# Kernel optimization log

Hardware: AMD Instinct MI355X
Metric: run time of the kernel (lower is better)

Reference implementation:

```python
import jax, jax.numpy as jnp
import numpy as np

B, T, E = 2, 2048, 1024
H = 16            # num_heads (global in source repo)
D = E // H        # head_len
LN_EPS = 1e-5


def setup_inputs() -> dict:
    key = jax.random.key(0)
    ks = jax.random.split(key, 12)
    s = lambda fan_in: 1.0 / np.sqrt(fan_in)
    return {
        "x":     jax.random.normal(ks[0], (B, T, E), jnp.float32),
        "ln1_g": jnp.ones((E,), jnp.float32),
        "ln1_b": jnp.zeros((E,), jnp.float32),
        "Wq":    jax.random.normal(ks[1], (E, E), jnp.float32) * s(E),
        "Wk":    jax.random.normal(ks[2], (E, E), jnp.float32) * s(E),
        "Wv":    jax.random.normal(ks[3], (E, E), jnp.float32) * s(E),
        "Wo":    jax.random.normal(ks[4], (E, E), jnp.float32) * s(E),
        "bo":    jnp.zeros((E,), jnp.float32),
        "ln2_g": jnp.ones((E,), jnp.float32),
        "ln2_b": jnp.zeros((E,), jnp.float32),
        "W1":    jax.random.normal(ks[5], (E, 4 * E), jnp.float32) * s(E),
        "b1":    jnp.zeros((4 * E,), jnp.float32),
        "W2":    jax.random.normal(ks[6], (4 * E, E), jnp.float32) * s(4 * E),
        "b2":    jnp.zeros((E,), jnp.float32),
    }


def _layernorm(x, g, b):
    mu = jnp.mean(x, axis=-1, keepdims=True)
    var = jnp.mean(jnp.square(x - mu), axis=-1, keepdims=True)
    return (x - mu) * jax.lax.rsqrt(var + LN_EPS) * g + b


def _attention(x, Wq, Wk, Wv, Wo, bo):
    b, t, e = x.shape
    q = (x @ Wq).reshape(b, t, H, D)
    k = (x @ Wk).reshape(b, t, H, D)
    v = (x @ Wv).reshape(b, t, H, D)
    scores = jnp.einsum("bqhd,bkhd->bhqk", q, k) / np.sqrt(D).astype(np.float32)
    causal = jnp.tril(jnp.ones((t, t), bool))
    scores = jnp.where(causal, scores, -jnp.inf)
    attn = jax.nn.softmax(scores, axis=-1)
    out = jnp.einsum("bhqk,bkhd->bqhd", attn, v).reshape(b, t, e)
    return out @ Wo + bo


def reference(x, ln1_g, ln1_b, Wq, Wk, Wv, Wo, bo, ln2_g, ln2_b, W1, b1, W2, b2):
    # pre-norm attention + residual (dropout=0 / eval mode)
    x = x + _attention(_layernorm(x, ln1_g, ln1_b), Wq, Wk, Wv, Wo, bo)
    # pre-norm MLP + residual
    h = _layernorm(x, ln2_g, ln2_b)
    h = jax.nn.relu(h @ W1 + b1) @ W2 + b2
    return x + h
```

## Files before the change

### kernel.cpp

```cpp
#include <hip/hip_runtime.h>
#include <cmath>
#include <cstdint>
#include <cstddef>

typedef __bf16 bf16_t;
typedef _Float16 f16_t;
typedef __bf16 bf16x8 __attribute__((ext_vector_type(8)));
typedef float  f32x4  __attribute__((ext_vector_type(4)));

#define B_   2
#define T_   2048
#define E_   1024
#define H_   16
#define D_   64
#define FF_  4096
#define NROW (B_ * T_)
#define QS_  (3 * E_)
#define NTI  (T_ / 64)

__device__ __forceinline__ float4 ld4h(const f16_t* p)
{
    union { ushort4 u; f16_t h[4]; } c;
    c.u = *(const ushort4*)p;
    return make_float4((float)c.h[0], (float)c.h[1], (float)c.h[2], (float)c.h[3]);
}

__global__ __launch_bounds__(256) void ln_kernel(
    const float* __restrict__ x, const float* __restrict__ g,
    const float* __restrict__ bta, bf16_t* __restrict__ out)
{
    int row = blockIdx.x;
    int tid = threadIdx.x;
    const float4* xr = (const float4*)(x + (size_t)row * E_);
    float4 v = xr[tid];
    float s  = v.x + v.y + v.z + v.w;
    float ss = v.x * v.x + v.y * v.y + v.z * v.z + v.w * v.w;
#pragma unroll
    for (int off = 32; off; off >>= 1) {
        s  += __shfl_xor(s, off);
        ss += __shfl_xor(ss, off);
    }
    __shared__ float red[8];
    int wave = tid >> 6, lane = tid & 63;
    if (lane == 0) { red[wave] = s; red[4 + wave] = ss; }
    __syncthreads();
    s  = red[0] + red[1] + red[2] + red[3];
    ss = red[4] + red[5] + red[6] + red[7];
    float mu   = s * (1.0f / E_);
    float var  = ss * (1.0f / E_) - mu * mu;
    float rstd = rsqrtf(var + 1e-5f);
    float4 gv = ((const float4*)g)[tid];
    float4 bv = ((const float4*)bta)[tid];
    union { bf16_t h[4]; ushort4 u; } pk;
    pk.h[0] = (bf16_t)((v.x - mu) * rstd * gv.x + bv.x);
    pk.h[1] = (bf16_t)((v.y - mu) * rstd * gv.y + bv.y);
    pk.h[2] = (bf16_t)((v.z - mu) * rstd * gv.z + bv.z);
    pk.h[3] = (bf16_t)((v.w - mu) * rstd * gv.w + bv.w);
    ((ushort4*)(out + (size_t)row * E_))[tid] = pk.u;
}

__global__ __launch_bounds__(256) void ln_reduce2(
    const f16_t* __restrict__ p, const float* __restrict__ bias,
    const float* __restrict__ resid, float* __restrict__ x1,
    const float* __restrict__ g, const float* __restrict__ bta,
    bf16_t* __restrict__ out)
{
    int row = blockIdx.x;
    int tid = threadIdx.x;
    size_t off = (size_t)row * E_;
    float4 v0 = ld4h(p + off + tid * 4);
    float4 v1 = ld4h(p + (size_t)NROW * E_ + off + tid * 4);
    float4 bb = ((const float4*)bias)[tid];
    float4 rr = ((const float4*)(resid + off))[tid];
    float4 v;
    v.x = v0.x + v1.x + bb.x + rr.x;
    v.y = v0.y + v1.y + bb.y + rr.y;
    v.z = v0.z + v1.z + bb.z + rr.z;
    v.w = v0.w + v1.w + bb.w + rr.w;
    ((float4*)(x1 + off))[tid] = v;
    float s  = v.x + v.y + v.z + v.w;
    float ss = v.x * v.x + v.y * v.y + v.z * v.z + v.w * v.w;
#pragma unroll
    for (int o = 32; o; o >>= 1) {
        s  += __shfl_xor(s, o);
        ss += __shfl_xor(ss, o);
    }
    __shared__ float red[8];
    int wave = tid >> 6, lane = tid & 63;
    if (lane == 0) { red[wave] = s; red[4 + wave] = ss; }
    __syncthreads();
    s  = red[0] + red[1] + red[2] + red[3];
    ss = red[4] + red[5] + red[6] + red[7];
    float mu   = s * (1.0f / E_);
    float var  = ss * (1.0f / E_) - mu * mu;
    float rstd = rsqrtf(var + 1e-5f);
    float4 gv = ((const float4*)g)[tid];
    float4 bv = ((const float4*)bta)[tid];
    union { bf16_t h[4]; ushort4 u; } pk;
    pk.h[0] = (bf16_t)((v.x - mu) * rstd * gv.x + bv.x);
    pk.h[1] = (bf16_t)((v.y - mu) * rstd * gv.y + bv.y);
    pk.h[2] = (bf16_t)((v.z - mu) * rstd * gv.z + bv.z);
    pk.h[3] = (bf16_t)((v.w - mu) * rstd * gv.w + bv.w);
    ((ushort4*)(out + off))[tid] = pk.u;
}

__global__ __launch_bounds__(256) void add_reduce4(
    const f16_t* __restrict__ p, const float* __restrict__ bias,
    const float* __restrict__ resid, float* __restrict__ out)
{
    int row = blockIdx.x;
    int tid = threadIdx.x;
    size_t off = (size_t)row * E_ + tid * 4;
    const size_t MN = (size_t)NROW * E_;
    float4 v0 = ld4h(p + off);
    float4 v1 = ld4h(p + MN + off);
    float4 v2 = ld4h(p + 2 * MN + off);
    float4 v3 = ld4h(p + 3 * MN + off);
    float4 bb = ((const float4*)bias)[tid];
    float4 rr = ((const float4*)(resid + (size_t)row * E_))[tid];
    float4 v;
    v.x = (v0.x + v1.x) + (v2.x + v3.x) + bb.x + rr.x;
    v.y = (v0.y + v1.y) + (v2.y + v3.y) + bb.y + rr.y;
    v.z = (v0.z + v1.z) + (v2.z + v3.z) + bb.z + rr.z;
    v.w = (v0.w + v1.w) + (v2.w + v3.w) + bb.w + rr.w;
    ((float4*)(out + (size_t)row * E_))[tid] = v;
}

__global__ __launch_bounds__(256) void transpose_all(
    const float* __restrict__ Wq, const float* __restrict__ Wk,
    const float* __restrict__ Wv, const float* __restrict__ Wo,
    const float* __restrict__ W1, const float* __restrict__ W2,
    bf16_t* __restrict__ wqkv, bf16_t* __restrict__ wot,
    bf16_t* __restrict__ w1t, bf16_t* __restrict__ w2t)
{
    int l = blockIdx.x;
    const float* W; bf16_t* Wt; int K, N, bx, by;
    if (l < 4096) {
        int seg = l >> 10, r = l & 1023;
        K = E_; N = E_; bx = r & 31; by = r >> 5;
        if      (seg == 0) { W = Wq; Wt = wqkv; }
        else if (seg == 1) { W = Wk; Wt = wqkv + (size_t)E_ * E_; }
        else if (seg == 2) { W = Wv; Wt = wqkv + (size_t)2 * E_ * E_; }
        else               { W = Wo; Wt = wot; }
    } else if (l < 8192) {
        int r = l - 4096; K = E_; N = FF_; bx = r & 127; by = r >> 7;
        W = W1; Wt = w1t;
    } else {
        int r = l - 8192; K = FF_; N = E_; bx = r & 31; by = r >> 5;
        W = W2; Wt = w2t;
    }
    __shared__ float t[32][33];
    int n0 = bx * 32, k0 = by * 32;
    int tx = threadIdx.x & 31, ty = threadIdx.x >> 5;
#pragma unroll
    for (int i = 0; i < 4; ++i)
        t[ty + i * 8][tx] = W[(size_t)(k0 + ty + i * 8) * N + n0 + tx];
    __syncthreads();
#pragma unroll
    for (int i = 0; i < 4; ++i)
        Wt[(size_t)(n0 + ty + i * 8) * K + k0 + tx] = (bf16_t)t[tx][ty + i * 8];
}

__device__ __forceinline__ void gload16(const bf16_t* g, bf16_t* l)
{
    __builtin_amdgcn_global_load_lds(
        (const __attribute__((address_space(1))) void*)g,
        (__attribute__((address_space(3))) void*)l, 16, 0, 0);
}

#define BM 128
#define BN 128
#define BK 64

__global__ __launch_bounds__(256) void gemm_bt(
    const bf16_t* __restrict__ A, const bf16_t* __restrict__ Bt,
    const float* __restrict__ bias, const float* __restrict__ resid,
    void* __restrict__ Cout, bf16_t* __restrict__ vt_out,
    int M, int N, int K, int lda, int ldb,
    int has_bias, int do_relu, int has_resid, int out_bf16)
{
    __shared__ __attribute__((aligned(16))) bf16_t As[BM * BK];
    __shared__ __attribute__((aligned(16))) bf16_t Bs[BN * BK];
    int tid  = threadIdx.x;
    int lane = tid & 63, wave = tid >> 6;
    int gx = gridDim.x, nwg = gx * gridDim.y;
    int orig = blockIdx.y * gx + blockIdx.x;
    int wg = (orig & 7) * (nwg >> 3) + (orig >> 3);
    int m0 = (wg % gx) * BM, n0 = (wg / gx) * BN;
    int wm = (wave & 1) * 64, wn = (wave >> 1) * 64;
    int koff = blockIdx.z * K;
    f32x4 acc[4][4];
#pragma unroll
    for (int i = 0; i < 4; ++i)
#pragma unroll
        for (int j = 0; j < 4; ++j) acc[i][j] = (f32x4){0.f, 0.f, 0.f, 0.f};

    const int ml = lane & 15;
    const int g  = lane >> 4;
    const int swl = ml & 7;

    int r8 = lane >> 3;
    int scw = ((lane & 7) ^ r8) * 8;
    const bf16_t* Ag = A  + (size_t)(m0 + wave * 32 + r8) * lda + koff + scw;
    const bf16_t* Bg = Bt + (size_t)(n0 + wave * 32 + r8) * ldb + koff + scw;
    bf16_t* Asw = &As[wave * 32 * BK];
    bf16_t* Bsw = &Bs[wave * 32 * BK];
    int niter = K / BK;

#pragma unroll
    for (int j = 0; j < 4; ++j) {
        gload16(Ag + (size_t)j * 8 * lda, Asw + j * 8 * BK);
        gload16(Bg + (size_t)j * 8 * ldb, Bsw + j * 8 * BK);
    }

    const char* Ac = (const char*)As;
    const char* Bc = (const char*)Bs;
    for (int it = 0; it < niter; ++it) {
        __syncthreads();
#pragma unroll
        for (int ks = 0; ks < 2; ++ks) {
            int swc = (((ks << 2) + g) ^ swl) << 4;
            bf16x8 af[4], bfr[4];
#pragma unroll
            for (int mi = 0; mi < 4; ++mi)
                af[mi] = *(const bf16x8*)(Ac + (wm + mi * 16 + ml) * 128 + swc);
#pragma unroll
            for (int ni = 0; ni < 4; ++ni)
                bfr[ni] = *(const bf16x8*)(Bc + (wn + ni * 16 + ml) * 128 + swc);
#pragma unroll
            for (int mi = 0; mi < 4; ++mi)
#pragma unroll
                for (int ni = 0; ni < 4; ++ni)
                    acc[mi][ni] = __builtin_amdgcn_mfma_f32_16x16x32_bf16(
                        af[mi], bfr[ni], acc[mi][ni], 0, 0, 0);
        }
        if (it + 1 < niter) {
            __syncthreads();
            int k0 = (it + 1) * BK;
#pragma unroll
            for (int j = 0; j < 4; ++j) {
                gload16(Ag + k0 + (size_t)j * 8 * lda, Asw + j * 8 * BK);
                gload16(Bg + k0 + (size_t)j * 8 * ldb, Bsw + j * 8 * BK);
            }
        }
    }

    int r4 = (lane >> 4) * 4;
    if (gridDim.z > 1) {
        f16_t* P = (f16_t*)Cout + (size_t)blockIdx.z * M * N;
#pragma unroll
        for (int mi = 0; mi < 4; ++mi)
#pragma unroll
            for (int ni = 0; ni < 4; ++ni) {
                int col = n0 + wn + ni * 16 + ml;
#pragma unroll
                for (int r = 0; r < 4; ++r) {
                    int row = m0 + wm + mi * 16 + r4 + r;
                    P[(size_t)row * N + col] = (f16_t)acc[mi][ni][r];
                }
            }
        return;
    }
#pragma unroll
    for (int mi = 0; mi < 4; ++mi) {
#pragma unroll
        for (int ni = 0; ni < 4; ++ni) {
            int col = n0 + wn + ni * 16 + ml;
            float bval = has_bias ? bias[col] : 0.0f;
#pragma unroll
            for (int r = 0; r < 4; ++r) {
                int row = m0 + wm + mi * 16 + r4 + r;
                float v = acc[mi][ni][r] + bval;
                if (do_relu)   v = fmaxf(v, 0.0f);
                if (has_resid) v += resid[(size_t)row * N + col];
                if (out_bf16)
                    ((bf16_t*)Cout)[(size_t)row * N + col] = (bf16_t)v;
                else
                    ((float*)Cout)[(size_t)row * N + col] = v;
            }
        }
    }
}

__device__ __forceinline__ void g256_stage_half(
    const bf16_t* gbase, int ldg, bf16_t* lhalf, int wave, int lane)
{
    int r = lane >> 3, c = lane & 7;
    int sc = (c ^ r) * 8;
#pragma unroll
    for (int j = 0; j < 2; ++j) {
        const bf16_t* src = gbase + (size_t)(wave * 8 + j * 64 + r) * ldg + sc;
        bf16_t* dst = lhalf + (wave * 8 + j * 64) * 64;
        __builtin_amdgcn_global_load_lds(
            (const __attribute__((address_space(1))) void*)src,
            (__attribute__((address_space(3))) void*)dst, 16, 0, 0);
    }
}

__device__ __forceinline__ bf16x8 g256_frag(const bf16_t* half, int row, int kb)
{
    return *(const bf16x8*)((const char*)half + row * 128 + (kb ^ ((row & 7) << 4)));
}

template<int FP, bool DO_BFR>
__device__ __forceinline__ void g256_reads(
    const bf16_t* Ahx, const bf16_t* Bhx,
    bf16x8 (&af)[2][2], bf16x8 (&bfr)[4][2],
    int ml, int kq16, int brow0)
{
    if (DO_BFR) {
#pragma unroll
        for (int ni = 0; ni < 4; ++ni) {
            bfr[ni][0] = g256_frag(Bhx, brow0 + ni * 16 + ml, kq16);
            bfr[ni][1] = g256_frag(Bhx, brow0 + ni * 16 + ml, 64 + kq16);
        }
    }
#pragma unroll
    for (int i = 0; i < 2; ++i) {
        af[i][0] = g256_frag(Ahx, (2 * FP + i) * 16 + ml, kq16);
        af[i][1] = g256_frag(Ahx, (2 * FP + i) * 16 + ml, 64 + kq16);
    }
}

template<int FP>
__device__ __forceinline__ void g256_mfma(
    const bf16x8 (&af)[2][2], const bf16x8 (&bfr)[4][2], f32x4 (&acc)[8][4])
{
    __builtin_amdgcn_s_setprio(1);
#pragma unroll
    for (int i = 0; i < 2; ++i)
#pragma unroll
        for (int ni = 0; ni < 4; ++ni)
#pragma unroll
            for (int ks = 0; ks < 2; ++ks)
                acc[2 * FP + i][ni] = __builtin_amdgcn_mfma_f32_16x16x32_bf16(
                    af[i][ks], bfr[ni][ks], acc[2 * FP + i][ni], 0, 0, 0);
    __builtin_amdgcn_s_setprio(0);
}

#define AHALF(t, h) (ldsr + ((((t) & 1) * 4 + (h)) * (128 * 64)))
#define BHALF(t, h) (ldsr + ((((t) & 1) * 4 + 2 + (h)) * (128 * 64)))
#define STG_A(t, h) g256_stage_half(Ab + (size_t)((h) * 128) * lda + (t) * 64, lda, AHALF(t, h), wave, lane)
#define STG_B(t, h) g256_stage_half(Bb + (size_t)((h) * 128) * ldb + (t) * 64, ldb, BHALF(t, h), wave, lane)
#define SBAR() __builtin_amdgcn_s_barrier()

__global__ __launch_bounds__(512, 2) void gemm256(
    const bf16_t* __restrict__ A, const bf16_t* __restrict__ Bt,
    const float* __restrict__ bias,
    void* __restrict__ Cout, bf16_t* __restrict__ vt_out,
    int M, int N, int K, int lda, int ldb,
    int has_bias, int do_relu, int split)
{
    extern __shared__ __attribute__((aligned(16))) bf16_t ldsr[];
    int tid = threadIdx.x, lane = tid & 63, wave = tid >> 6;
    int gx = gridDim.x, nwg = gx * gridDim.y;
    int orig = blockIdx.y * gx + blockIdx.x;
    int wg = (orig & 7) * (nwg >> 3) + (orig >> 3);
    int m0 = (wg % gx) * 256, n0 = (wg / gx) * 256;
    int koff = blockIdx.z * K;
    int ml = lane & 15, kq16 = (lane >> 4) * 16, r4 = (lane >> 4) * 4;
    int wr = (wave >> 2) * 128, wc = (wave & 3) * 64;
    int brow0 = (wave & 1) * 64;

    const bf16_t* Ab = A  + (size_t)m0 * lda + koff;
    const bf16_t* Bb = Bt + (size_t)n0 * ldb + koff;

    const bf16_t* A0 = AHALF(0, wave >> 2);
    const bf16_t* A1 = AHALF(1, wave >> 2);
    const bf16_t* B0 = BHALF(0, (wave & 3) >> 1);
    const bf16_t* B1 = BHALF(1, (wave & 3) >> 1);

    f32x4 acc[8][4];
#pragma unroll
    for (int i = 0; i < 8; ++i)
#pragma unroll
        for (int j = 0; j < 4; ++j) acc[i][j] = (f32x4){0.f, 0.f, 0.f, 0.f};
    bf16x8 bfr[4][2];

    STG_B(0, 0); STG_B(0, 1);
    STG_A(0, 0); STG_A(0, 1);
    STG_B(1, 0); STG_B(1, 1);
    asm volatile("s_waitcnt vmcnt(4)" ::: "memory");
    SBAR();

    int NIT2 = K / 128;
    for (int it = 0; it < NIT2; ++it) {
        bool last = (it == NIT2 - 1);
        int t1 = 2 * it + 1, t2 = 2 * it + 2, t3 = 2 * it + 3;
        bf16x8 af[2][2];

        g256_reads<0, true>(A0, B0, af, bfr, ml, kq16, brow0);
        STG_A(t1, 0);
        SBAR();
        g256_mfma<0>(af, bfr, acc);
        SBAR();

        g256_reads<1, false>(A0, B0, af, bfr, ml, kq16, brow0);
        STG_A(t1, 1);
        SBAR();
        g256_mfma<1>(af, bfr, acc);
        SBAR();

        g256_reads<2, false>(A0, B0, af, bfr, ml, kq16, brow0);
        if (!last) STG_B(t2, 0);
        SBAR();
        g256_mfma<2>(af, bfr, acc);
        SBAR();

        g256_reads<3, false>(A0, B0, af, bfr, ml, kq16, brow0);
        if (!last) STG_B(t2, 1);
        SBAR();
        g256_mfma<3>(af, bfr, acc);
        if (last) asm volatile("s_waitcnt vmcnt(0)" ::: "memory");
        else      asm volatile("s_waitcnt vmcnt(4)" ::: "memory");
        SBAR();

        g256_reads<0, true>(A1, B1, af, bfr, ml, kq16, brow0);
        if (!last) STG_A(t2, 0);
        SBAR();
        g256_mfma<0>(af, bfr, acc);
        SBAR();

        g256_reads<1, false>(A1, B1, af, bfr, ml, kq16, brow0);
        if (!last) STG_A(t2, 1);
        SBAR();
        g256_mfma<1>(af, bfr, acc);
        SBAR();

        g256_reads<2, false>(A1, B1, af, bfr, ml, kq16, brow0);
        if (!last) STG_B(t3, 0);
        SBAR();
        g256_mfma<2>(af, bfr, acc);
        SBAR();

        g256_reads<3, false>(A1, B1, af, bfr, ml, kq16, brow0);
        if (!last) STG_B(t3, 1);
        SBAR();
        g256_mfma<3>(af, bfr, acc);
        if (!last) asm volatile("s_waitcnt vmcnt(4)" ::: "memory");
        SBAR();
    }

    if (split > 1) {
        f16_t* P = (f16_t*)Cout + (size_t)blockIdx.z * M * N;
#pragma unroll
        for (int mi = 0; mi < 8; ++mi)
#pragma unroll
            for (int ni = 0; ni < 4; ++ni) {
                int col = n0 + wc + ni * 16 + ml;
#pragma unroll
                for (int r = 0; r < 4; ++r) {
                    int row = m0 + wr + mi * 16 + r4 + r;
                    P[(size_t)row * N + col] = (f16_t)acc[mi][ni][r];
                }
            }
        return;
    }
    if (vt_out && n0 >= 2 * E_) {
#pragma unroll
        for (int mi = 0; mi < 8; ++mi)
#pragma unroll
            for (int ni = 0; ni < 4; ++ni) {
                int vcol = n0 + wc + ni * 16 + ml - 2 * E_;
                int h = vcol >> 6, d = vcol & 63;
                int row0 = m0 + wr + mi * 16 + r4;
                int b = row0 >> 11, t = row0 & (T_ - 1);
                union { bf16_t h4[4]; uint2 u; } pk;
#pragma unroll
                for (int r = 0; r < 4; ++r) pk.h4[r] = (bf16_t)acc[mi][ni][r];
                *(uint2*)&vt_out[((size_t)(b * H_ + h) * D_ + d) * T_ + t] = pk.u;
            }
        return;
    }
#pragma unroll
    for (int mi = 0; mi < 8; ++mi) {
#pragma unroll
        for (int ni = 0; ni < 4; ++ni) {
            int col = n0 + wc + ni * 16 + ml;
            float bval = has_bias ? bias[col] : 0.0f;
#pragma unroll
            for (int r = 0; r < 4; ++r) {
                int row = m0 + wr + mi * 16 + r4 + r;
                float v = acc[mi][ni][r] + bval;
                if (do_relu) v = fmaxf(v, 0.0f);
                ((bf16_t*)Cout)[(size_t)row * N + col] = (bf16_t)v;
            }
        }
    }
}

#define PSTR 72
#define QSCL 0.1803368801111204f

__device__ __forceinline__ float exp2_hw(float x)
{
    float r;
    asm("v_exp_f32 %0, %1" : "=v"(r) : "v"(x));
    return r;
}

struct TileState {
    f32x4 acc[4];
    float l1;
};

__device__ __forceinline__ void attn_stage8(
    const bf16_t* kb, const bf16_t* vb,
    bf16_t* ksl, bf16_t* vsl, int wave, int lane)
{
    int r = lane >> 3;
    int sc = ((lane & 7) ^ r) * 8;
    int rb = wave * 8;
    gload16(kb + (size_t)(rb + r) * QS_ + sc, ksl + rb * 64);
    gload16(vb + (size_t)(rb + r) * T_  + sc, vsl + rb * 64);
}

__device__ __forceinline__ void tile_update(
    const bf16x8 kf[2][4], const bf16x8 vf[2][4], const bf16x8 qf[2],
    TileState& st, bf16_t* PsW, int ml, int r4, int kq8,
    bool diag, int ch, int qrow)
{
    f32x4 s[4];
    __builtin_amdgcn_s_setprio(1);
#pragma unroll
    for (int nt = 0; nt < 4; ++nt) {
        s[nt] = (f32x4){0.f, 0.f, 0.f, 0.f};
#pragma unroll
        for (int ks = 0; ks < 2; ++ks)
            s[nt] = __builtin_amdgcn_mfma_f32_16x16x32_bf16(kf[ks][nt], qf[ks], s[nt], 0, 0, 0);
    }
    __builtin_amdgcn_s_setprio(0);
    if (diag) {
#pragma unroll
        for (int nt = 0; nt < 4; ++nt)
#pragma unroll
            for (int r = 0; r < 4; ++r)
                if (ch * 64 + nt * 16 + r4 + r > qrow) s[nt][r] = -INFINITY;
    }
    float sum = 0.f;
#pragma unroll
    for (int nt = 0; nt < 4; ++nt)
#pragma unroll
        for (int r = 0; r < 4; ++r) {
            float p = exp2_hw(s[nt][r]);
            s[nt][r] = p;
            sum += p;
        }
    st.l1 += sum;

#pragma unroll
    for (int nt = 0; nt < 4; ++nt) {
        union { bf16_t h[4]; uint2 u; } pk;
#pragma unroll
        for (int r = 0; r < 4; ++r) pk.h[r] = (bf16_t)s[nt][r];
        *(uint2*)&PsW[ml * PSTR + nt * 16 + r4] = pk.u;
    }
    __builtin_amdgcn_s_setprio(1);
#pragma unroll
    for (int ks = 0; ks < 2; ++ks) {
        bf16x8 pf = *(const bf16x8*)&PsW[ml * PSTR + ks * 32 + kq8];
#pragma unroll
        for (int dt = 0; dt < 4; ++dt)
            st.acc[dt] = __builtin_amdgcn_mfma_f32_16x16x32_bf16(vf[ks][dt], pf, st.acc[dt], 0, 0, 0);
    }
    __builtin_amdgcn_s_setprio(0);
}

__global__ __launch_bounds__(512, 4) void attn_mfma(
    const bf16_t* __restrict__ Qp, const bf16_t* __restrict__ Kp,
    const bf16_t* __restrict__ Vt, bf16_t* __restrict__ O)
{
    __shared__ __attribute__((aligned(16))) bf16_t Ks[2][64 * 64];
    __shared__ __attribute__((aligned(16))) bf16_t Vts[2][64 * 64];
    __shared__ __attribute__((aligned(16))) bf16_t Ps[8][16 * PSTR];

    int tid = threadIdx.x, lane = tid & 63, wave = tid >> 6;
    int ml  = lane & 15;
    int kq8 = (lane >> 4) * 8;
    int g   = lane >> 4;
    int r4  = (lane >> 4) * 4;
    int swl = ml & 7;
    int bh = blockIdx.y, b = bh >> 4, h = bh & 15;
    size_t qk_base = (size_t)b * T_ * QS_ + h * D_;
    size_t vt_base = (size_t)bh * D_ * T_;
    size_t o_base  = (size_t)b * T_ * E_ + h * D_;

    int lo = blockIdx.x, hi = NTI - 1 - blockIdx.x;
    int half = wave >> 2, w4 = wave & 3;
    int qtile = half ? lo : hi;
    int qw = qtile * 64 + w4 * 16;

    bf16x8 qf[2];
#pragma unroll
    for (int ks = 0; ks < 2; ++ks) {
        bf16x8 a = *(const bf16x8*)&Qp[qk_base + (size_t)(qw + ml) * QS_ + ks * 32 + kq8];
#pragma unroll
        for (int j = 0; j < 8; ++j)
            a[j] = (bf16_t)((float)a[j] * QSCL);
        qf[ks] = a;
    }

    TileState st;
#pragma unroll
    for (int dt = 0; dt < 4; ++dt)
        st.acc[dt] = (f32x4){0.f, 0.f, 0.f, 0.f};
    st.l1 = 0.f;

    int nch = hi + 1;

    attn_stage8(Kp + qk_base, Vt + vt_base, Ks[0], Vts[0], wave, lane);

    for (int ch = 0; ch < nch; ++ch) {
        int cur = ch & 1, nxt = cur ^ 1;
        __syncthreads();

        if (ch + 1 < nch)
            attn_stage8(Kp + qk_base + (size_t)((ch + 1) * 64) * QS_,
                        Vt + vt_base + (ch + 1) * 64,
                        Ks[nxt], Vts[nxt], wave, lane);

        if (ch <= qtile) {
            bf16x8 kf[2][4], vf[2][4];
            const char* kc = (const char*)Ks[cur];
            const char* vc = (const char*)Vts[cur];
#pragma unroll
            for (int ks = 0; ks < 2; ++ks) {
                int swc = (((ks << 2) + g) ^ swl) << 4;
#pragma unroll
                for (int nt = 0; nt < 4; ++nt) {
                    int off = (nt * 16 + ml) * 128 + swc;
                    kf[ks][nt] = *(const bf16x8*)(kc + off);
                    vf[ks][nt] = *(const bf16x8*)(vc + off);
                }
            }
            tile_update(kf, vf, qf, st, Ps[wave], ml, r4, kq8,
                        ch == qtile, ch, qw + ml);
        }
    }

    {
        float l1 = st.l1;
        l1 += __shfl_xor(l1, 16);
        l1 += __shfl_xor(l1, 32);
        float inv = 1.0f / l1;
        bf16_t* PsW = Ps[wave];
#pragma unroll
        for (int dt = 0; dt < 4; ++dt) {
            union { bf16_t h[4]; uint2 u; } pk;
#pragma unroll
            for (int r = 0; r < 4; ++r) pk.h[r] = (bf16_t)(st.acc[dt][r] * inv);
            *(uint2*)&PsW[ml * PSTR + dt * 16 + r4] = pk.u;
        }
        int row = lane >> 2, seg = (lane & 3) * 16;
        bf16x8 o0 = *(const bf16x8*)&PsW[row * PSTR + seg];
        bf16x8 o1 = *(const bf16x8*)&PsW[row * PSTR + seg + 8];
        size_t gp = o_base + (size_t)(qw + row) * E_ + seg;
        *(bf16x8*)&O[gp]     = o0;
        *(bf16x8*)&O[gp + 8] = o1;
    }
}

extern "C" void kernel_launch(void* const* d_in, const int* in_sizes, int n_in,
                              void* d_out, int out_size, void* d_ws, size_t ws_size,
                              hipStream_t stream)
{
    const float* x    = (const float*)d_in[0];
    const float* ln1g = (const float*)d_in[1];
    const float* ln1b = (const float*)d_in[2];
    const float* Wq   = (const float*)d_in[3];
    const float* Wk   = (const float*)d_in[4];
    const float* Wv   = (const float*)d_in[5];
    const float* Wo   = (const float*)d_in[6];
    const float* bo   = (const float*)d_in[7];
    const float* ln2g = (const float*)d_in[8];
    const float* ln2b = (const float*)d_in[9];
    const float* W1   = (const float*)d_in[10];
    const float* b1   = (const float*)d_in[11];
    const float* W2   = (const float*)d_in[12];
    const float* b2   = (const float*)d_in[13];

    char* ws = (char*)d_ws;
    const size_t MB = 1024ull * 1024ull;
    bf16_t* w2t     = (bf16_t*)(ws + 0 * MB);
    float*  x1      = (float*)(ws + 8 * MB);
    f16_t*  part_wo = (f16_t*)(ws + 24 * MB);
    bf16_t* h1      = (bf16_t*)(ws + 24 * MB);
    bf16_t* w1t     = (bf16_t*)(ws + 56 * MB);
    bf16_t* xn      = (bf16_t*)(ws + 64 * MB);
    bf16_t* hb      = (bf16_t*)(ws + 64 * MB);
    bf16_t* wqkv    = (bf16_t*)(ws + 72 * MB);
    bf16_t* wot     = (bf16_t*)(ws + 78 * MB);
    bf16_t* QKV     = (bf16_t*)(ws + 80 * MB);
    bf16_t* Vtb     = (bf16_t*)(ws + 104 * MB);
    bf16_t* att     = (bf16_t*)(ws + 112 * MB);
    f16_t*  part4   = (f16_t*)(ws + 56 * MB);

    dim3 blk(256), blk5(512);
    const size_t LDS256 = 8 * 128 * 64 * sizeof(bf16_t);

    transpose_all<<<dim3(12288), blk, 0, stream>>>(
        Wq, Wk, Wv, Wo, W1, W2, wqkv, wot, w1t, w2t);

    ln_kernel<<<dim3(NROW), blk, 0, stream>>>(x, ln1g, ln1b, xn);

    gemm256<<<dim3(NROW / 256, QS_ / 256, 1), blk5, LDS256, stream>>>(
        xn, wqkv, nullptr, QKV, Vtb, NROW, QS_, E_, E_, E_, 0, 0, 1);

    attn_mfma<<<dim3(NTI / 2, B_ * H_), dim3(512), 0, stream>>>(
        QKV, QKV + E_, Vtb, att);

    gemm_bt<<<dim3(NROW / BM, E_ / BN, 2), blk, 0, stream>>>(
        att, wot, nullptr, nullptr, part_wo, nullptr, NROW, E_, E_ / 2, E_, E_, 0, 0, 0, 0);
    ln_reduce2<<<dim3(NROW), blk, 0, stream>>>(
        part_wo, bo, x, x1, ln2g, ln2b, hb);

    gemm256<<<dim3(NROW / 256, FF_ / 256, 1), blk5, LDS256, stream>>>(
        hb, w1t, b1, h1, nullptr, NROW, FF_, E_, E_, E_, 1, 1, 1);

    gemm256<<<dim3(NROW / 256, E_ / 256, 4), blk5, LDS256, stream>>>(
        h1, w2t, nullptr, part4, nullptr, NROW, E_, FF_ / 4, FF_, FF_, 0, 0, 4);
    add_reduce4<<<dim3(NROW), blk, 0, stream>>>(
        part4, b2, x1, (float*)d_out);
}
```

Baseline: 309.5 us.

## Process two query sub-tiles per wave in attention, halving block size

The attention kernel now runs 4 waves per block instead of 8, with each wave handling two 16-row query sub-tiles. K and V fragments loaded from LDS are reused across both sub-tiles, which halves LDS fragment reads per query row. K/V staging is widened so each wave loads 16 rows, and the Ps scratch is indexed per sub-tile. This costs more registers per wave (two accumulator sets) and gives fewer waves per block to hide latency; the launch bound no longer requests a minimum occupancy.

```diff
diff --git a/kernel.cpp b/kernel.cpp
--- a/kernel.cpp
+++ b/kernel.cpp
@@ -504,15 +504,17 @@
     float l1;
 };
 
-__device__ __forceinline__ void attn_stage8(
+__device__ __forceinline__ void attn_stage4(
     const bf16_t* kb, const bf16_t* vb,
     bf16_t* ksl, bf16_t* vsl, int wave, int lane)
 {
     int r = lane >> 3;
     int sc = ((lane & 7) ^ r) * 8;
-    int rb = wave * 8;
-    gload16(kb + (size_t)(rb + r) * QS_ + sc, ksl + rb * 64);
-    gload16(vb + (size_t)(rb + r) * T_  + sc, vsl + rb * 64);
+    int rb = wave * 16;
+    gload16(kb + (size_t)(rb + r) * QS_ + sc,     ksl + rb * 64);
+    gload16(kb + (size_t)(rb + 8 + r) * QS_ + sc, ksl + (rb + 8) * 64);
+    gload16(vb + (size_t)(rb + r) * T_ + sc,      vsl + rb * 64);
+    gload16(vb + (size_t)(rb + 8 + r) * T_ + sc,  vsl + (rb + 8) * 64);
 }
 
 __device__ __forceinline__ void tile_update(
@@ -566,7 +568,7 @@
     __builtin_amdgcn_s_setprio(0);
 }
 
-__global__ __launch_bounds__(512, 4) void attn_mfma(
+__global__ __launch_bounds__(256) void attn_mfma(
     const bf16_t* __restrict__ Qp, const bf16_t* __restrict__ Kp,
     const bf16_t* __restrict__ Vt, bf16_t* __restrict__ O)
 {
@@ -586,36 +588,41 @@
     size_t o_base  = (size_t)b * T_ * E_ + h * D_;
 
     int lo = blockIdx.x, hi = NTI - 1 - blockIdx.x;
-    int half = wave >> 2, w4 = wave & 3;
+    int half = wave >> 1, sub = wave & 1;
     int qtile = half ? lo : hi;
-    int qw = qtile * 64 + w4 * 16;
-
-    bf16x8 qf[2];
+    int qw0 = qtile * 64 + sub * 32;
+
+    bf16x8 qf0[2], qf1[2];
 #pragma unroll
     for (int ks = 0; ks < 2; ++ks) {
-        bf16x8 a = *(const bf16x8*)&Qp[qk_base + (size_t)(qw + ml) * QS_ + ks * 32 + kq8];
-#pragma unroll
-        for (int j = 0; j < 8; ++j)
+        bf16x8 a = *(const bf16x8*)&Qp[qk_base + (size_t)(qw0 + ml) * QS_ + ks * 32 + kq8];
+        bf16x8 c = *(const bf16x8*)&Qp[qk_base + (size_t)(qw0 + 16 + ml) * QS_ + ks * 32 + kq8];
+#pragma unroll
+        for (int j = 0; j < 8; ++j) {
             a[j] = (bf16_t)((float)a[j] * QSCL);
-        qf[ks] = a;
-    }
-
-    TileState st;
-#pragma unroll
-    for (int dt = 0; dt < 4; ++dt)
-        st.acc[dt] = (f32x4){0.f, 0.f, 0.f, 0.f};
-    st.l1 = 0.f;
+            c[j] = (bf16_t)((float)c[j] * QSCL);
+        }
+        qf0[ks] = a; qf1[ks] = c;
+    }
+
+    TileState st0, st1;
+#pragma unroll
+    for (int dt = 0; dt < 4; ++dt) {
+        st0.acc[dt] = (f32x4){0.f, 0.f, 0.f, 0.f};
+        st1.acc[dt] = (f32x4){0.f, 0.f, 0.f, 0.f};
+    }
+    st0.l1 = 0.f; st1.l1 = 0.f;
 
     int nch = hi + 1;
 
-    attn_stage8(Kp + qk_base, Vt + vt_base, Ks[0], Vts[0], wave, lane);
+    attn_stage4(Kp + qk_base, Vt + vt_base, Ks[0], Vts[0], wave, lane);
 
     for (int ch = 0; ch < nch; ++ch) {
         int cur = ch & 1, nxt = cur ^ 1;
         __syncthreads();
 
         if (ch + 1 < nch)
-            attn_stage8(Kp + qk_base + (size_t)((ch + 1) * 64) * QS_,
+            attn_stage4(Kp + qk_base + (size_t)((ch + 1) * 64) * QS_,
                         Vt + vt_base + (ch + 1) * 64,
                         Ks[nxt], Vts[nxt], wave, lane);
 
@@ -633,17 +640,23 @@
                     vf[ks][nt] = *(const bf16x8*)(vc + off);
                 }
             }
-            tile_update(kf, vf, qf, st, Ps[wave], ml, r4, kq8,
-                        ch == qtile, ch, qw + ml);
-        }
-    }
-
-    {
+            bool dg = (ch == qtile);
+            tile_update(kf, vf, qf0, st0, Ps[2 * wave], ml, r4, kq8,
+                        dg, ch, qw0 + ml);
+            tile_update(kf, vf, qf1, st1, Ps[2 * wave + 1], ml, r4, kq8,
+                        dg, ch, qw0 + 16 + ml);
+        }
+    }
+
+#pragma unroll
+    for (int t = 0; t < 2; ++t) {
+        TileState& st = t ? st1 : st0;
+        int qwt = qw0 + t * 16;
+        bf16_t* PsW = Ps[2 * wave + t];
         float l1 = st.l1;
         l1 += __shfl_xor(l1, 16);
         l1 += __shfl_xor(l1, 32);
         float inv = 1.0f / l1;
-        bf16_t* PsW = Ps[wave];
 #pragma unroll
         for (int dt = 0; dt < 4; ++dt) {
             union { bf16_t h[4]; uint2 u; } pk;
@@ -654,7 +667,7 @@
         int row = lane >> 2, seg = (lane & 3) * 16;
         bf16x8 o0 = *(const bf16x8*)&PsW[row * PSTR + seg];
         bf16x8 o1 = *(const bf16x8*)&PsW[row * PSTR + seg + 8];
-        size_t gp = o_base + (size_t)(qw + row) * E_ + seg;
+        size_t gp = o_base + (size_t)(qwt + row) * E_ + seg;
         *(bf16x8*)&O[gp]     = o0;
         *(bf16x8*)&O[gp + 8] = o1;
     }
@@ -706,7 +719,7 @@
     gemm256<<<dim3(NROW / 256, QS_ / 256, 1), blk5, LDS256, stream>>>(
         xn, wqkv, nullptr, QKV, Vtb, NROW, QS_, E_, E_, E_, 0, 0, 1);
 
-    attn_mfma<<<dim3(NTI / 2, B_ * H_), dim3(512), 0, stream>>>(
+    attn_mfma<<<dim3(NTI / 2, B_ * H_), blk, 0, stream>>>(
         QKV, QKV + E_, Vtb, att);
 
     gemm_bt<<<dim3(NROW / BM, E_ / BN, 2), blk, 0, stream>>>(
```

New measurement: 326.2 us. 1.05x slower.
